# Performance work log

Measured on AMD Instinct MI355X. Metric: run time of the kernel, lower is better.

## Reference

```python
import jax, jax.numpy as jnp
import numpy as np

# Directional rectangle cumulative max: max over the axis-aligned rectangle
# between each pixel and one image corner.

def _rectmax(x, rev_h, rev_w):
    y = jax.lax.cummax(x, axis=2, reverse=rev_h)
    return jax.lax.cummax(y, axis=3, reverse=rev_w)


def _guided_pool(xq, gq, rev_h, rev_w):
    # Guided landmark pool: each pixel takes max of itself and the directional
    # cumulative max restricted to guide==1 positions. With guide == ones this
    # reduces to the plain directional rectangle cummax (the un-guided pool).
    neg = jnp.finfo(xq.dtype).min
    masked = jnp.where(gq > 0, xq, neg)
    return jnp.maximum(xq, _rectmax(masked, rev_h, rev_w))

# (rev_h, rev_w) for TopLeft, TopRight, BottomLeft, BottomRight pools
_DIRS = [(True, True), (True, False), (False, True), (False, False)]


def setup_inputs() -> dict:
    key = jax.random.key(0)
    k1, k2, k3 = jax.random.split(key, 3)
    B, C, H, W = 16, 256, 64, 64
    Cout, K = 256, 3
    x = jax.random.normal(k1, (B, C, H, W), jnp.float32)
    weight = jax.random.normal(k2, (Cout, C, K, K), jnp.float32) * 0.02
    bias = jax.random.normal(k3, (Cout,), jnp.float32) * 0.02
    return {"x": x, "weight": weight, "bias": bias}


def reference(x, weight, bias):
    B, C, H, W = x.shape
    Q = C // 4
    # Original torch code squares x IN PLACE via chunk() views before pooling.
    xsq = x * x
    # Per-quadrant channel energy and its global (row, col) argmax -> one-hot guide.
    energy = xsq.reshape(B, 4, Q, H, W).sum(axis=2)            # [B,4,H,W]
    idx = jnp.argmax(energy.reshape(B, 4, H * W), axis=-1)     # [B,4]
    onehot = (jnp.arange(H * W) == idx[..., None]).astype(x.dtype)
    guide = jnp.broadcast_to(onehot.reshape(B, 4, 1, H, W), (B, 4, Q, H, W)).reshape(B, C, H, W)
    # Four directional guided pools, one per channel quadrant, then conv.
    xs = jnp.split(xsq, 4, axis=1)
    gs = jnp.split(guide, 4, axis=1)
    pooled = jnp.concatenate(
        [_guided_pool(xs[i], gs[i], *_DIRS[i]) for i in range(4)], axis=1)
    out = jax.lax.conv_general_dilated(
        pooled, weight, window_strides=(1, 1), padding='SAME',
        dimension_numbers=('NCHW', 'OIHW', 'NCHW'))
    return out + bias[None, :, None, None]
```

## Files before the change

### kernel.cpp

```cpp
#include <hip/hip_runtime.h>
#include <cstddef>

#define B_   16
#define C_   256
#define HW_  4096

typedef __attribute__((ext_vector_type(8)))  short bf16x8;
typedef __attribute__((ext_vector_type(16))) float f32x16;

static __device__ __forceinline__ unsigned short f2bf(float f) {
    unsigned int u = __float_as_uint(f);
    u += 0x7fffu + ((u >> 16) & 1u);
    return (unsigned short)(u >> 16);
}

__global__ __launch_bounds__(256) void fused_energy(const float* __restrict__ x,
                                                    unsigned short* __restrict__ xsqN,
                                                    float* __restrict__ pval,
                                                    int* __restrict__ pidx) {
    int blk = blockIdx.x;
    int b = blk >> 6, h = blk & 63;
    int tid = threadIdx.x;
    int w = tid & 63, layer = tid >> 6;
    __shared__ float earr[4][4][64];
    __shared__ unsigned short tile[64][264];
    float e0 = 0.f, e1 = 0.f, e2 = 0.f, e3 = 0.f;
    const float* xb = x + (size_t)b * C_ * HW_ + h * 64 + w;
#pragma unroll
    for (int i = 0; i < 8; ++i) {
        int c0 = (i * 4 + layer) * 8;
        union { unsigned short us[8]; int4 v; } u;
        float es = 0.f;
#pragma unroll
        for (int k = 0; k < 8; ++k) {
            float v = xb[(size_t)(c0 + k) * HW_];
            float s = v * v;
            es += s;
            u.us[k] = f2bf(s);
        }
        *(int4*)&tile[w][c0] = u.v;
        if ((i >> 1) == 0) e0 += es;
        else if ((i >> 1) == 1) e1 += es;
        else if ((i >> 1) == 2) e2 += es;
        else e3 += es;
    }
    earr[layer][0][w] = e0; earr[layer][1][w] = e1;
    earr[layer][2][w] = e2; earr[layer][3][w] = e3;
    __syncthreads();
    size_t base = (size_t)(b * 64 + h) * 64 * 256;
#pragma unroll
    for (int it = 0; it < 8; ++it) {
        int row  = it * 8 + (tid >> 5);
        int col8 = (tid & 31) * 8;
        *(int4*)(xsqN + base + (size_t)row * 256 + col8) = *(int4*)&tile[row][col8];
    }
    int q = tid >> 6;
    float ev = earr[0][q][w] + earr[1][q][w] + earr[2][q][w] + earr[3][q][w];
    int ix = h * 64 + w;
#pragma unroll
    for (int off = 32; off; off >>= 1) {
        float ov = __shfl_down(ev, off);
        int   oi = __shfl_down(ix, off);
        if (ov > ev || (ov == ev && oi < ix)) { ev = ov; ix = oi; }
    }
    if ((tid & 63) == 0) {
        pval[(b * 64 + h) * 4 + q] = ev;
        pidx[(b * 64 + h) * 4 + q] = ix;
    }
}

__global__ __launch_bounds__(64) void energy_final(const float* __restrict__ pval,
                                                   const int* __restrict__ pidx,
                                                   int* __restrict__ lm) {
    int bq = blockIdx.x;
    int b = bq >> 2, q = bq & 3;
    int h = threadIdx.x;
    float ev = pval[(b * 64 + h) * 4 + q];
    int   ix = pidx[(b * 64 + h) * 4 + q];
#pragma unroll
    for (int off = 32; off; off >>= 1) {
        float ov = __shfl_down(ev, off);
        int   oi = __shfl_down(ix, off);
        if (ov > ev || (ov == ev && oi < ix)) { ev = ov; ix = oi; }
    }
    if (h == 0) lm[bq] = ix;
}

__global__ __launch_bounds__(256) void lval_kernel(const unsigned short* __restrict__ xsqN,
                                                   const int* __restrict__ lm,
                                                   unsigned short* __restrict__ Lval) {
    int t = blockIdx.x * 256 + threadIdx.x;
    int b = t >> 8, c = t & 255, q = c >> 6;
    int l = lm[b * 4 + q];
    Lval[t] = xsqN[((size_t)((b * 64 + (l >> 6)) * 64 + (l & 63))) * 256 + c];
}

__global__ __launch_bounds__(64) void wt_pack(const float* __restrict__ w,
                                              unsigned short* __restrict__ wa) {
    int blk  = blockIdx.x;
    int lane = threadIdx.x;
    int cog = blk & 7;
    int s   = (blk >> 3) & 1;
    int cib = (blk >> 4) & 7;
    int j   = blk >> 7;
    int co  = cog * 32 + (lane & 31);
    int k0  = cib * 32 + s * 16 + (lane >> 5) * 8;
    union { unsigned short us[8]; int4 v; } u;
#pragma unroll
    for (int jj = 0; jj < 8; ++jj) {
        int ci = k0 + jj;
        u.us[jj] = f2bf(w[(size_t)(co * 256 + ci) * 9 + j]);
    }
    *(int4*)(wa + ((size_t)blk * 64 + lane) * 8) = u.v;
}

__global__ __launch_bounds__(512, 2) void conv_mfma(const unsigned short* __restrict__ xsqN,
                                                    const unsigned short* __restrict__ wa,
                                                    const float* __restrict__ bias,
                                                    const int* __restrict__ lm,
                                                    const unsigned short* __restrict__ Lval,
                                                    float* __restrict__ out) {
    int pt = blockIdx.x;
    int b  = pt >> 4;
    int h0 = (pt & 15) * 4;
    int tid  = threadIdx.x;
    int lane = tid & 63;
    int wv   = tid >> 6;
    int wy = wv >> 2, wx = wv & 3;
    int l31 = lane & 31, qh = lane >> 5;

    __shared__ unsigned short Bs[2][6 * 66 * 40];

    f32x16 acc[4][2];
#pragma unroll
    for (int mt = 0; mt < 4; ++mt)
#pragma unroll
        for (int nt = 0; nt < 2; ++nt)
#pragma unroll
            for (int r = 0; r < 16; ++r) acc[mt][nt][r] = 0.f;

    int4 sv[4];

    {
#pragma unroll
        for (int t2 = 0; t2 < 4; ++t2) {
            int idx = tid + t2 * 512;
            int4 v = {0, 0, 0, 0};
            if (idx < 1584) {
                int pr = idx / 264; int rem = idx - pr * 264;
                int pc = rem >> 2;  int part = rem & 3;
                int grow = h0 - 1 + pr, gcol = pc - 1;
                if ((unsigned)grow < 64u && (unsigned)gcol < 64u)
                    v = *(const int4*)(xsqN + (((size_t)(b * 64 + grow) * 64 + gcol) * 256 + part * 8));
            }
            sv[t2] = v;
        }
        int l = lm[b * 4 + 0];
        int hm = l >> 6, wm = l & 63;
#pragma unroll
        for (int t2 = 0; t2 < 4; ++t2) {
            int idx = tid + t2 * 512;
            if (idx < 1584) {
                int pr = idx / 264; int rem = idx - pr * 264;
                int pc = rem >> 2;  int part = rem & 3;
                int grow = h0 - 1 + pr, gcol = pc - 1;
                union { int4 v; unsigned short us[8]; } u; u.v = sv[t2];
                bool inb = ((unsigned)grow < 64u) && ((unsigned)gcol < 64u);
                if (inb && grow <= hm && gcol <= wm) {
                    union { int4 v; unsigned short us[8]; } Lu;
                    Lu.v = *(const int4*)(Lval + b * 256 + part * 8);
#pragma unroll
                    for (int k = 0; k < 8; ++k)
                        if (Lu.us[k] > u.us[k]) u.us[k] = Lu.us[k];
                }
                *(int4*)(&Bs[0][(pr * 66 + pc) * 40 + part * 8]) = u.v;
            }
        }
    }
    __syncthreads();

    const bf16x8* Abase = (const bf16x8*)wa + (wy << 8) + lane;

    bf16x8 areg[2][4];
    {
        const bf16x8* Ap = Abase;
        areg[0][0] = Ap[0];
        areg[0][1] = Ap[64];
        areg[0][2] = Ap[128];
        areg[0][3] = Ap[192];
    }

    for (int cib = 0; cib < 8; ++cib) {
        const unsigned short* Bb = &Bs[cib & 1][0];
        const bf16x8* Ac = Abase + ((size_t)cib << 10);

#pragma unroll
        for (int j = 0; j < 9; ++j) {
            int j3 = j / 3;
            int r  = wx + j3;
            int w0 = l31 + (j - j3 * 3);
            const unsigned short* Bp = Bb + (r * 66 + w0) * 40 + qh * 8;
#pragma unroll
            for (int s = 0; s < 2; ++s) {
                const int h = j * 2 + s;
                const int pb = h & 1;

                if (h < 17) {
                    const int hn = h + 1;
                    const int jn = hn >> 1, sn = hn & 1;
                    const bf16x8* Ap = Ac + (size_t)jn * 8192 + (sn << 9);
                    areg[pb ^ 1][0] = Ap[0];
                    areg[pb ^ 1][1] = Ap[64];
                    areg[pb ^ 1][2] = Ap[128];
                    areg[pb ^ 1][3] = Ap[192];
                } else if (cib < 7) {
                    const bf16x8* Ap = Abase + ((size_t)(cib + 1) << 10);
                    areg[pb ^ 1][0] = Ap[0];
                    areg[pb ^ 1][1] = Ap[64];
                    areg[pb ^ 1][2] = Ap[128];
                    areg[pb ^ 1][3] = Ap[192];
                }

                if (h == 1 && cib < 7) {
                    int nc = cib + 1;
#pragma unroll
                    for (int t2 = 0; t2 < 4; ++t2) {
                        int idx = tid + t2 * 512;
                        int4 v = {0, 0, 0, 0};
                        if (idx < 1584) {
                            int pr = idx / 264; int rem = idx - pr * 264;
                            int pc = rem >> 2;  int part = rem & 3;
                            int grow = h0 - 1 + pr, gcol = pc - 1;
                            if ((unsigned)grow < 64u && (unsigned)gcol < 64u)
                                v = *(const int4*)(xsqN + (((size_t)(b * 64 + grow) * 64 + gcol) * 256 + nc * 32 + part * 8));
                        }
                        sv[t2] = v;
                    }
                }

                bf16x8 b0 = *(const bf16x8*)(Bp + s * 16);
                bf16x8 b1 = *(const bf16x8*)(Bp + 1280 + s * 16);

                acc[0][0] = __builtin_amdgcn_mfma_f32_32x32x16_bf16(areg[pb][0], b0, acc[0][0], 0, 0, 0);
                acc[0][1] = __builtin_amdgcn_mfma_f32_32x32x16_bf16(areg[pb][0], b1, acc[0][1], 0, 0, 0);
                acc[1][0] = __builtin_amdgcn_mfma_f32_32x32x16_bf16(areg[pb][1], b0, acc[1][0], 0, 0, 0);
                acc[1][1] = __builtin_amdgcn_mfma_f32_32x32x16_bf16(areg[pb][1], b1, acc[1][1], 0, 0, 0);
                acc[2][0] = __builtin_amdgcn_mfma_f32_32x32x16_bf16(areg[pb][2], b0, acc[2][0], 0, 0, 0);
                acc[2][1] = __builtin_amdgcn_mfma_f32_32x32x16_bf16(areg[pb][2], b1, acc[2][1], 0, 0, 0);
                acc[3][0] = __builtin_amdgcn_mfma_f32_32x32x16_bf16(areg[pb][3], b0, acc[3][0], 0, 0, 0);
                acc[3][1] = __builtin_amdgcn_mfma_f32_32x32x16_bf16(areg[pb][3], b1, acc[3][1], 0, 0, 0);
            }
        }

        if (cib < 7) {
            int nc = cib + 1;
            int l = lm[b * 4 + (nc >> 1)];
            int hm = l >> 6, wm = l & 63;
            bool qhle = (nc >> 1) < 2;
            bool qwle = ((nc >> 1) & 1) == 0;
            unsigned short* Bw = &Bs[(cib + 1) & 1][0];
#pragma unroll
            for (int t2 = 0; t2 < 4; ++t2) {
                int idx = tid + t2 * 512;
                if (idx < 1584) {
                    int pr = idx / 264; int rem = idx - pr * 264;
                    int pc = rem >> 2;  int part = rem & 3;
                    int grow = h0 - 1 + pr, gcol = pc - 1;
                    union { int4 v; unsigned short us[8]; } u; u.v = sv[t2];
                    bool inb = ((unsigned)grow < 64u) && ((unsigned)gcol < 64u);
                    bool hok = qhle ? (grow <= hm) : (grow >= hm);
                    bool wok = qwle ? (gcol <= wm) : (gcol >= wm);
                    if (inb && hok && wok) {
                        union { int4 v; unsigned short us[8]; } Lu;
                        Lu.v = *(const int4*)(Lval + b * 256 + nc * 32 + part * 8);
#pragma unroll
                        for (int k = 0; k < 8; ++k)
                            if (Lu.us[k] > u.us[k]) u.us[k] = Lu.us[k];
                    }
                    *(int4*)(&Bw[(pr * 66 + pc) * 40 + part * 8]) = u.v;
                }
            }
        }
        __syncthreads();
    }

    int h = h0 + wx;
#pragma unroll
    for (int mt = 0; mt < 4; ++mt) {
#pragma unroll
        for (int nt = 0; nt < 2; ++nt) {
#pragma unroll
            for (int r = 0; r < 16; ++r) {
                int row = (r & 3) + 8 * (r >> 2) + 4 * qh;
                int co  = wy * 128 + mt * 32 + row;
                int w   = nt * 32 + l31;
                out[(((size_t)(b * 256 + co)) * 64 + h) * 64 + w] = acc[mt][nt][r] + bias[co];
            }
        }
    }
}

extern "C" void kernel_launch(void* const* d_in, const int* in_sizes, int n_in,
                              void* d_out, int out_size, void* d_ws, size_t ws_size,
                              hipStream_t stream) {
    const float* x      = (const float*)d_in[0];
    const float* weight = (const float*)d_in[1];
    const float* bias   = (const float*)d_in[2];
    float* out = (float*)d_out;

    char* ws = (char*)d_ws;
    int*            lmp  = (int*)ws;
    float*          pval = (float*)(ws + 256);
    int*            pidx = (int*)(ws + 256 + 16384);
    unsigned short* Lval = (unsigned short*)(ws + 256 + 32768);
    unsigned short* Wa   = (unsigned short*)(ws + 49152);
    unsigned short* xsqN = (unsigned short*)(ws + 49152 + 1179648);

    hipLaunchKernelGGL(fused_energy, dim3(1024), dim3(256), 0, stream, x, xsqN, pval, pidx);
    hipLaunchKernelGGL(energy_final, dim3(64), dim3(64), 0, stream, pval, pidx, lmp);
    hipLaunchKernelGGL(lval_kernel, dim3(16), dim3(256), 0, stream, xsqN, lmp, Lval);
    hipLaunchKernelGGL(wt_pack, dim3(1152), dim3(64), 0, stream, weight, Wa);
    hipLaunchKernelGGL(conv_mfma, dim3(256), dim3(512), 0, stream, xsqN, Wa, bias, lmp, Lval, out);
}
```

Before: 213.8 us.

## Split conv output channels across two blocks, single-buffer LDS, raise occupancy

The conv kernel now launches twice as many blocks, each computing half of the output channels (64 per wave instead of 128), which halves the accumulator registers. LDS drops to a single buffer and the A operand double-buffering and register prefetch of the next B tile are removed, in favour of sync-stage-sync between channel blocks. Launch bounds ask for 4 blocks per CU so more waves can hide latency. The trade-off is that each input tile is staged twice (once per channel half), and loads no longer overlap with MFMA inside a block.

```diff
diff --git a/kernel.cpp b/kernel.cpp
--- a/kernel.cpp
+++ b/kernel.cpp
@@ -114,185 +114,121 @@
     *(int4*)(wa + ((size_t)blk * 64 + lane) * 8) = u.v;
 }
 
-__global__ __launch_bounds__(512, 2) void conv_mfma(const unsigned short* __restrict__ xsqN,
+static __device__ __forceinline__ void stage_B(unsigned short* __restrict__ Bs,
+                                               const unsigned short* __restrict__ xsqN,
+                                               const unsigned short* __restrict__ Lval,
+                                               const int* __restrict__ lm,
+                                               int b, int h0, int nc, int tid) {
+    int l = lm[b * 4 + (nc >> 1)];
+    int hm = l >> 6, wm = l & 63;
+    bool qhle = (nc >> 1) < 2;
+    bool qwle = ((nc >> 1) & 1) == 0;
+    int4 sv[4];
+#pragma unroll
+    for (int t2 = 0; t2 < 4; ++t2) {
+        int idx = tid + t2 * 512;
+        int4 v = {0, 0, 0, 0};
+        if (idx < 1584) {
+            int pr = idx / 264; int rem = idx - pr * 264;
+            int pc = rem >> 2;  int part = rem & 3;
+            int grow = h0 - 1 + pr, gcol = pc - 1;
+            if ((unsigned)grow < 64u && (unsigned)gcol < 64u)
+                v = *(const int4*)(xsqN + (((size_t)(b * 64 + grow) * 64 + gcol) * 256 + nc * 32 + part * 8));
+        }
+        sv[t2] = v;
+    }
+#pragma unroll
+    for (int t2 = 0; t2 < 4; ++t2) {
+        int idx = tid + t2 * 512;
+        if (idx < 1584) {
+            int pr = idx / 264; int rem = idx - pr * 264;
+            int pc = rem >> 2;  int part = rem & 3;
+            int grow = h0 - 1 + pr, gcol = pc - 1;
+            union { int4 v; unsigned short us[8]; } u; u.v = sv[t2];
+            bool inb = ((unsigned)grow < 64u) && ((unsigned)gcol < 64u);
+            bool hok = qhle ? (grow <= hm) : (grow >= hm);
+            bool wok = qwle ? (gcol <= wm) : (gcol >= wm);
+            if (inb && hok && wok) {
+                union { int4 v; unsigned short us[8]; } Lu;
+                Lu.v = *(const int4*)(Lval + b * 256 + nc * 32 + part * 8);
+#pragma unroll
+                for (int k = 0; k < 8; ++k)
+                    if (Lu.us[k] > u.us[k]) u.us[k] = Lu.us[k];
+            }
+            *(int4*)(&Bs[(pr * 66 + pc) * 40 + part * 8]) = u.v;
+        }
+    }
+}
+
+__global__ __launch_bounds__(512, 4) void conv_mfma(const unsigned short* __restrict__ xsqN,
                                                     const unsigned short* __restrict__ wa,
                                                     const float* __restrict__ bias,
                                                     const int* __restrict__ lm,
                                                     const unsigned short* __restrict__ Lval,
                                                     float* __restrict__ out) {
-    int pt = blockIdx.x;
-    int b  = pt >> 4;
-    int h0 = (pt & 15) * 4;
+    int pt   = blockIdx.x;
+    int ch   = pt >> 8;
+    int tile = pt & 255;
+    int b    = tile >> 4;
+    int h0   = (tile & 15) * 4;
     int tid  = threadIdx.x;
     int lane = tid & 63;
     int wv   = tid >> 6;
     int wy = wv >> 2, wx = wv & 3;
     int l31 = lane & 31, qh = lane >> 5;
-
-    __shared__ unsigned short Bs[2][6 * 66 * 40];
-
-    f32x16 acc[4][2];
-#pragma unroll
-    for (int mt = 0; mt < 4; ++mt)
+    int cq  = ch * 2 + wy;
+
+    __shared__ unsigned short Bs[6 * 66 * 40];
+
+    f32x16 acc[2][2];
+#pragma unroll
+    for (int mt = 0; mt < 2; ++mt)
 #pragma unroll
         for (int nt = 0; nt < 2; ++nt)
 #pragma unroll
             for (int r = 0; r < 16; ++r) acc[mt][nt][r] = 0.f;
 
-    int4 sv[4];
-
-    {
-#pragma unroll
-        for (int t2 = 0; t2 < 4; ++t2) {
-            int idx = tid + t2 * 512;
-            int4 v = {0, 0, 0, 0};
-            if (idx < 1584) {
-                int pr = idx / 264; int rem = idx - pr * 264;
-                int pc = rem >> 2;  int part = rem & 3;
-                int grow = h0 - 1 + pr, gcol = pc - 1;
-                if ((unsigned)grow < 64u && (unsigned)gcol < 64u)
-                    v = *(const int4*)(xsqN + (((size_t)(b * 64 + grow) * 64 + gcol) * 256 + part * 8));
-            }
-            sv[t2] = v;
-        }
-        int l = lm[b * 4 + 0];
-        int hm = l >> 6, wm = l & 63;
-#pragma unroll
-        for (int t2 = 0; t2 < 4; ++t2) {
-            int idx = tid + t2 * 512;
-            if (idx < 1584) {
-                int pr = idx / 264; int rem = idx - pr * 264;
-                int pc = rem >> 2;  int part = rem & 3;
-                int grow = h0 - 1 + pr, gcol = pc - 1;
-                union { int4 v; unsigned short us[8]; } u; u.v = sv[t2];
-                bool inb = ((unsigned)grow < 64u) && ((unsigned)gcol < 64u);
-                if (inb && grow <= hm && gcol <= wm) {
-                    union { int4 v; unsigned short us[8]; } Lu;
-                    Lu.v = *(const int4*)(Lval + b * 256 + part * 8);
-#pragma unroll
-                    for (int k = 0; k < 8; ++k)
-                        if (Lu.us[k] > u.us[k]) u.us[k] = Lu.us[k];
-                }
-                *(int4*)(&Bs[0][(pr * 66 + pc) * 40 + part * 8]) = u.v;
-            }
-        }
-    }
+    stage_B(Bs, xsqN, Lval, lm, b, h0, 0, tid);
     __syncthreads();
 
-    const bf16x8* Abase = (const bf16x8*)wa + (wy << 8) + lane;
-
-    bf16x8 areg[2][4];
-    {
-        const bf16x8* Ap = Abase;
-        areg[0][0] = Ap[0];
-        areg[0][1] = Ap[64];
-        areg[0][2] = Ap[128];
-        areg[0][3] = Ap[192];
-    }
+    const bf16x8* Abase = (const bf16x8*)wa + (cq << 7) + lane;
 
     for (int cib = 0; cib < 8; ++cib) {
-        const unsigned short* Bb = &Bs[cib & 1][0];
-        const bf16x8* Ac = Abase + ((size_t)cib << 10);
-
 #pragma unroll
         for (int j = 0; j < 9; ++j) {
             int j3 = j / 3;
             int r  = wx + j3;
             int w0 = l31 + (j - j3 * 3);
-            const unsigned short* Bp = Bb + (r * 66 + w0) * 40 + qh * 8;
+            const unsigned short* Bp = Bs + (r * 66 + w0) * 40 + qh * 8;
+            const bf16x8* Ap = Abase + (((size_t)(j * 8 + cib)) << 10);
 #pragma unroll
             for (int s = 0; s < 2; ++s) {
-                const int h = j * 2 + s;
-                const int pb = h & 1;
-
-                if (h < 17) {
-                    const int hn = h + 1;
-                    const int jn = hn >> 1, sn = hn & 1;
-                    const bf16x8* Ap = Ac + (size_t)jn * 8192 + (sn << 9);
-                    areg[pb ^ 1][0] = Ap[0];
-                    areg[pb ^ 1][1] = Ap[64];
-                    areg[pb ^ 1][2] = Ap[128];
-                    areg[pb ^ 1][3] = Ap[192];
-                } else if (cib < 7) {
-                    const bf16x8* Ap = Abase + ((size_t)(cib + 1) << 10);
-                    areg[pb ^ 1][0] = Ap[0];
-                    areg[pb ^ 1][1] = Ap[64];
-                    areg[pb ^ 1][2] = Ap[128];
-                    areg[pb ^ 1][3] = Ap[192];
-                }
-
-                if (h == 1 && cib < 7) {
-                    int nc = cib + 1;
-#pragma unroll
-                    for (int t2 = 0; t2 < 4; ++t2) {
-                        int idx = tid + t2 * 512;
-                        int4 v = {0, 0, 0, 0};
-                        if (idx < 1584) {
-                            int pr = idx / 264; int rem = idx - pr * 264;
-                            int pc = rem >> 2;  int part = rem & 3;
-                            int grow = h0 - 1 + pr, gcol = pc - 1;
-                            if ((unsigned)grow < 64u && (unsigned)gcol < 64u)
-                                v = *(const int4*)(xsqN + (((size_t)(b * 64 + grow) * 64 + gcol) * 256 + nc * 32 + part * 8));
-                        }
-                        sv[t2] = v;
-                    }
-                }
-
+                bf16x8 a0 = Ap[s * 512];
+                bf16x8 a1 = Ap[s * 512 + 64];
                 bf16x8 b0 = *(const bf16x8*)(Bp + s * 16);
                 bf16x8 b1 = *(const bf16x8*)(Bp + 1280 + s * 16);
-
-                acc[0][0] = __builtin_amdgcn_mfma_f32_32x32x16_bf16(areg[pb][0], b0, acc[0][0], 0, 0, 0);
-                acc[0][1] = __builtin_amdgcn_mfma_f32_32x32x16_bf16(areg[pb][0], b1, acc[0][1], 0, 0, 0);
-                acc[1][0] = __builtin_amdgcn_mfma_f32_32x32x16_bf16(areg[pb][1], b0, acc[1][0], 0, 0, 0);
-                acc[1][1] = __builtin_amdgcn_mfma_f32_32x32x16_bf16(areg[pb][1], b1, acc[1][1], 0, 0, 0);
-                acc[2][0] = __builtin_amdgcn_mfma_f32_32x32x16_bf16(areg[pb][2], b0, acc[2][0], 0, 0, 0);
-                acc[2][1] = __builtin_amdgcn_mfma_f32_32x32x16_bf16(areg[pb][2], b1, acc[2][1], 0, 0, 0);
-                acc[3][0] = __builtin_amdgcn_mfma_f32_32x32x16_bf16(areg[pb][3], b0, acc[3][0], 0, 0, 0);
-                acc[3][1] = __builtin_amdgcn_mfma_f32_32x32x16_bf16(areg[pb][3], b1, acc[3][1], 0, 0, 0);
+                acc[0][0] = __builtin_amdgcn_mfma_f32_32x32x16_bf16(a0, b0, acc[0][0], 0, 0, 0);
+                acc[0][1] = __builtin_amdgcn_mfma_f32_32x32x16_bf16(a0, b1, acc[0][1], 0, 0, 0);
+                acc[1][0] = __builtin_amdgcn_mfma_f32_32x32x16_bf16(a1, b0, acc[1][0], 0, 0, 0);
+                acc[1][1] = __builtin_amdgcn_mfma_f32_32x32x16_bf16(a1, b1, acc[1][1], 0, 0, 0);
             }
         }
-
         if (cib < 7) {
-            int nc = cib + 1;
-            int l = lm[b * 4 + (nc >> 1)];
-            int hm = l >> 6, wm = l & 63;
-            bool qhle = (nc >> 1) < 2;
-            bool qwle = ((nc >> 1) & 1) == 0;
-            unsigned short* Bw = &Bs[(cib + 1) & 1][0];
-#pragma unroll
-            for (int t2 = 0; t2 < 4; ++t2) {
-                int idx = tid + t2 * 512;
-                if (idx < 1584) {
-                    int pr = idx / 264; int rem = idx - pr * 264;
-                    int pc = rem >> 2;  int part = rem & 3;
-                    int grow = h0 - 1 + pr, gcol = pc - 1;
-                    union { int4 v; unsigned short us[8]; } u; u.v = sv[t2];
-                    bool inb = ((unsigned)grow < 64u) && ((unsigned)gcol < 64u);
-                    bool hok = qhle ? (grow <= hm) : (grow >= hm);
-                    bool wok = qwle ? (gcol <= wm) : (gcol >= wm);
-                    if (inb && hok && wok) {
-                        union { int4 v; unsigned short us[8]; } Lu;
-                        Lu.v = *(const int4*)(Lval + b * 256 + nc * 32 + part * 8);
-#pragma unroll
-                        for (int k = 0; k < 8; ++k)
-                            if (Lu.us[k] > u.us[k]) u.us[k] = Lu.us[k];
-                    }
-                    *(int4*)(&Bw[(pr * 66 + pc) * 40 + part * 8]) = u.v;
-                }
-            }
-        }
-        __syncthreads();
+            __syncthreads();
+            stage_B(Bs, xsqN, Lval, lm, b, h0, cib + 1, tid);
+            __syncthreads();
+        }
     }
 
     int h = h0 + wx;
 #pragma unroll
-    for (int mt = 0; mt < 4; ++mt) {
+    for (int mt = 0; mt < 2; ++mt) {
 #pragma unroll
         for (int nt = 0; nt < 2; ++nt) {
 #pragma unroll
             for (int r = 0; r < 16; ++r) {
                 int row = (r & 3) + 8 * (r >> 2) + 4 * qh;
-                int co  = wy * 128 + mt * 32 + row;
+                int co  = cq * 64 + mt * 32 + row;
                 int w   = nt * 32 + l31;
                 out[(((size_t)(b * 256 + co)) * 64 + h) * 64 + w] = acc[mt][nt][r] + bias[co];
             }
@@ -320,5 +256,5 @@
     hipLaunchKernelGGL(energy_final, dim3(64), dim3(64), 0, stream, pval, pidx, lmp);
     hipLaunchKernelGGL(lval_kernel, dim3(16), dim3(256), 0, stream, xsqN, lmp, Lval);
     hipLaunchKernelGGL(wt_pack, dim3(1152), dim3(64), 0, stream, weight, Wa);
-    hipLaunchKernelGGL(conv_mfma, dim3(256), dim3(512), 0, stream, xsqN, Wa, bias, lmp, Lval, out);
-}
+    hipLaunchKernelGGL(conv_mfma, dim3(512), dim3(512), 0, stream, xsqN, Wa, bias, lmp, Lval, out);
+}
```

Result: slower. 218.4 us (+2.1%).
